# Kernel optimization log

Measured on AMD Instinct MI355X. Metric: run time of the kernel, lower is better.

The kernel has to match this reference:

```python
import jax, jax.numpy as jnp
import numpy as np

EPS = 1e-12  # torch F.normalize eps

def _l2norm(v):
    return v / jnp.maximum(jnp.linalg.norm(v, axis=-1, keepdims=True), EPS)

def setup_inputs() -> dict:
    key = jax.random.key(0)
    x = jax.random.normal(key, (64, 64, 10, 512), dtype=jnp.float32)
    w = jnp.asarray(10.0, dtype=jnp.float32)
    b = jnp.asarray(-5.0, dtype=jnp.float32)
    return {"x": x, "w": w, "b": b}

def reference(x, w, b):
    B, N, M, D = x.shape
    NM = N * M
    x_flat = _l2norm(x.reshape(B, NM, D))                      # [B, NM, D]
    c_full = _l2norm(jnp.mean(x, axis=2))                      # [B, N, D]
    # leave-one-out centroid: (M * normalized_full_centroid - x) / (M - 1), then normalize
    c_excl = _l2norm(((M * c_full[:, :, None, :] - x) / (M - 1)).reshape(B, NM, D))  # [B, NM, D]
    # cosine sim of each utterance vs every (normalized) full centroid
    sim = jnp.einsum("bkd,bnd->bkn", x_flat, c_full)           # [B, NM, N]
    # replace own-speaker column with leave-one-out similarity (avoids [B,NM,N,D] blowup)
    excl_sim = jnp.sum(x_flat * c_excl, axis=-1)               # [B, NM]
    speaker_ids = jnp.repeat(jnp.arange(N), M)                 # [NM]
    rows = jnp.arange(NM)
    sim = sim.at[:, rows, speaker_ids].set(excl_sim)
    logits = w * sim + b                                       # [B, NM, N]
    logp = jax.nn.log_softmax(logits, axis=-1)
    # cross-entropy with targets = speaker_ids per row, mean over B*NM
    nll = -logp[:, rows, speaker_ids]                          # [B, NM]
    return jnp.mean(nll)
```

## Files before the change

kernel.cpp:

```cpp
#include <hip/hip_runtime.h>
#include <math.h>

static constexpr int Bn = 64;
static constexpr int Nn = 64;
static constexpr int Mn = 10;
static constexpr int Dn = 512;
static constexpr int NMn = Nn * Mn;
static constexpr int RT = 32;
static constexpr int NBLK2 = Bn * (NMn / RT);
static constexpr float EPSV = 1e-12f;

typedef unsigned short u16;
typedef unsigned int u32;
typedef __attribute__((ext_vector_type(8))) __bf16 bf16x8;
typedef __attribute__((ext_vector_type(4))) float f32x4;

static __device__ __forceinline__ u16 f2bf(float f) {
  u32 u = __float_as_uint(f);
  u = u + 0x7fffu + ((u >> 16) & 1u);
  return (u16)(u >> 16);
}


__global__ __launch_bounds__(256) void centroid_k(const float* __restrict__ x,
                                                  u16* __restrict__ ch2) {
  const int bn = blockIdx.x;
  const int tid = threadIdx.x;
  const int f4 = tid & 127;
  const int mg = tid >> 7;
  const int wv = tid >> 6, ln = tid & 63;
  const float4* xp = (const float4*)(x + (size_t)bn * (Mn * Dn));

  float4 a = {0.f, 0.f, 0.f, 0.f};
#pragma unroll
  for (int k = 0; k < 5; ++k) {
    const float4 v = xp[(2 * k + mg) * 128 + f4];
    a.x += v.x; a.y += v.y; a.z += v.z; a.w += v.w;
  }
  __shared__ float4 cred[128];
  if (mg == 1) cred[f4] = a;
  __syncthreads();

  float4 c = {0.f, 0.f, 0.f, 0.f};
  float cs = 0.f;
  if (mg == 0) {
    c = cred[f4];
    c.x += a.x; c.y += a.y; c.z += a.z; c.w += a.w;
    cs = c.x * c.x + c.y * c.y + c.z * c.z + c.w * c.w;
  }
#pragma unroll
  for (int t = 1; t < 64; t <<= 1) cs += __shfl_xor(cs, t, 64);
  __shared__ float csred[2];
  if (mg == 0 && ln == 0) csred[wv] = cs;
  __syncthreads();
  if (mg == 0) {
    const float scale = 1.0f / fmaxf(sqrtf(csred[0] + csred[1]), EPSV);
    const u16 h0 = f2bf(c.x * scale), h1 = f2bf(c.y * scale);
    const u16 h2 = f2bf(c.z * scale), h3 = f2bf(c.w * scale);
    uint2 w;
    w.x = (u32)h0 | ((u32)h1 << 16);
    w.y = (u32)h2 | ((u32)h3 << 16);
    const int n = bn & (Nn - 1), bb = bn >> 6;
    const size_t off = (((size_t)bb * 16 + (f4 >> 3)) * Nn + n) * 32 + ((f4 & 7) * 4);
    *(uint2*)(ch2 + off) = w;
  }
}

__global__ __launch_bounds__(512) void gemm_loss_k(const float* __restrict__ x,
                                                   const u16* __restrict__ ch2,
                                                   const float* __restrict__ wp,
                                                   const float* __restrict__ bp,
                                                   float* __restrict__ partial) {
  __shared__ float S[8][16][65];
  __shared__ float SQ[2][4][16];
  __shared__ float nred[8];

  const int b = blockIdx.x / (NMn / RT);
  const int rt = blockIdx.x % (NMn / RT);
  const int row0 = rt * RT;
  const int tid = threadIdx.x, wv = tid >> 6, ln = tid & 63;
  const int lr = ln & 15;
  const int lkb = (ln >> 4) * 8;
  const int rh = wv >> 2;
  const int q = wv & 3;
  const int k0 = q * 128;

  const float* arow = x + ((size_t)b * NMn + row0 + rh * 16 + lr) * Dn + k0 + lkb;
  const u16* brow = ch2 + (((size_t)b * 16 + q * 4) * Nn) * 32 + (size_t)lr * 32 + lkb;

  f32x4 acc0 = {0.f, 0.f, 0.f, 0.f};
  f32x4 acc1 = acc0, acc2 = acc0, acc3 = acc0;
  float sq = 0.f;

#pragma unroll
  for (int kk = 0; kk < 128; kk += 32) {
    const u16* bp8 = brow + (size_t)(kk >> 5) * (Nn * 32);
    const float4 f0 = *(const float4*)(arow + kk);
    const float4 f1 = *(const float4*)(arow + kk + 4);
    const bf16x8 b0 = *(const bf16x8*)(bp8);
    const bf16x8 b1 = *(const bf16x8*)(bp8 + 16 * 32);
    const bf16x8 b2 = *(const bf16x8*)(bp8 + 32 * 32);
    const bf16x8 b3 = *(const bf16x8*)(bp8 + 48 * 32);
    const float v[8] = {f0.x, f0.y, f0.z, f0.w, f1.x, f1.y, f1.z, f1.w};
    bf16x8 ah;
#pragma unroll
    for (int i = 0; i < 8; ++i) {
      ah[i] = (__bf16)v[i];
      sq = fmaf(v[i], v[i], sq);
    }
    acc0 = __builtin_amdgcn_mfma_f32_16x16x32_bf16(ah, b0, acc0, 0, 0, 0);
    acc1 = __builtin_amdgcn_mfma_f32_16x16x32_bf16(ah, b1, acc1, 0, 0, 0);
    acc2 = __builtin_amdgcn_mfma_f32_16x16x32_bf16(ah, b2, acc2, 0, 0, 0);
    acc3 = __builtin_amdgcn_mfma_f32_16x16x32_bf16(ah, b3, acc3, 0, 0, 0);
  }

  sq += __shfl_xor(sq, 16, 64);
  sq += __shfl_xor(sq, 32, 64);
  if (ln < 16) SQ[rh][q][lr] = sq;

  const int orow = (ln >> 4) * 4;
#pragma unroll
  for (int r = 0; r < 4; ++r) {
    S[wv][orow + r][lr] = acc0[r];
    S[wv][orow + r][16 + lr] = acc1[r];
    S[wv][orow + r][32 + lr] = acc2[r];
    S[wv][orow + r][48 + lr] = acc3[r];
  }
  __syncthreads();

  const float W = *wp, Bb = *bp;
  float acc_nll = 0.f;
#pragma unroll
  for (int i = 0; i < 4; ++i) {
    const int R = wv * 4 + i;
    const int rhh = R >> 4, rl = R & 15;
    const int krow = row0 + R;
    const int spk = krow / Mn;
    const float rn = S[rhh * 4 + 0][rl][ln] + S[rhh * 4 + 1][rl][ln] +
                     S[rhh * 4 + 2][rl][ln] + S[rhh * 4 + 3][rl][ln];
    const float x2 = SQ[rhh][0][rl] + SQ[rhh][1][rl] + SQ[rhh][2][rl] + SQ[rhh][3][rl];
    const float xn = sqrtf(x2);
    const float inv_xn = 1.0f / fmaxf(xn, EPSV);
    const float rspk = __shfl(rn, spk, 64);
    float sv = rn * inv_xn;
    if (ln == spk) {
      const float num = (float)Mn * rspk - x2;
      const float en = sqrtf(fmaxf((float)(Mn * Mn) - 2.0f * (float)Mn * rspk + x2, 0.f));
      sv = num / fmaxf(xn * en, EPSV);
    }
    const float logit = W * sv + Bb;
    const float lspk = __shfl(logit, spk, 64);
    float mx = logit;
#pragma unroll
    for (int t = 1; t < 64; t <<= 1) mx = fmaxf(mx, __shfl_xor(mx, t, 64));
    float se = expf(logit - mx);
#pragma unroll
    for (int t = 1; t < 64; t <<= 1) se += __shfl_xor(se, t, 64);
    acc_nll += (mx + logf(se)) - lspk;
  }
  if (ln == 0) nred[wv] = acc_nll;
  __syncthreads();
  if (tid == 0) {
    float s = 0.f;
#pragma unroll
    for (int i = 0; i < 8; ++i) s += nred[i];
    partial[blockIdx.x] = s;
  }
}

__global__ __launch_bounds__(256) void reduce_k(const float* __restrict__ partial,
                                                float* __restrict__ out) {
  const int tid = threadIdx.x;
  float s = 0.f;
  for (int i = tid; i < NBLK2; i += 256) s += partial[i];
#pragma unroll
  for (int t = 1; t < 64; t <<= 1) s += __shfl_xor(s, t, 64);
  __shared__ float red[4];
  if ((tid & 63) == 0) red[tid >> 6] = s;
  __syncthreads();
  if (tid == 0) out[0] = (red[0] + red[1] + red[2] + red[3]) * (1.0f / (float)(Bn * NMn));
}

static constexpr int ROWS = 8;
static constexpr int DCHUNK = 128;
static constexpr int CPAD = DCHUNK + 1;

__global__ __launch_bounds__(256) void centroid_fb_k(const float* __restrict__ x,
                                                     float* __restrict__ c) {
  const int bn = blockIdx.x;
  const float* xp = x + (size_t)bn * Mn * Dn;
  const int tid = threadIdx.x;
  float a0 = 0.f, a1 = 0.f;
#pragma unroll
  for (int m = 0; m < Mn; ++m) {
    a0 += xp[m * Dn + tid];
    a1 += xp[m * Dn + tid + 256];
  }
  float s = a0 * a0 + a1 * a1;
#pragma unroll
  for (int m = 1; m < 64; m <<= 1) s += __shfl_xor(s, m, 64);
  __shared__ float red[4];
  const int wv = tid >> 6, ln = tid & 63;
  if (ln == 0) red[wv] = s;
  __syncthreads();
  const float tot = red[0] + red[1] + red[2] + red[3];
  const float scale = 1.0f / fmaxf(sqrtf(tot), EPSV);
  float* cp = c + (size_t)bn * Dn;
  cp[tid] = a0 * scale;
  cp[tid + 256] = a1 * scale;
}

__global__ __launch_bounds__(256) void loss_fb_k(const float* __restrict__ x,
                                                 const float* __restrict__ c,
                                                 const float* __restrict__ wp,
                                                 const float* __restrict__ bp,
                                                 float* __restrict__ out) {
  __shared__ __align__(16) float x_lds[ROWS * Dn];
  __shared__ float c_lds[Nn * CPAD];
  __shared__ float xn2s[ROWS];
  __shared__ float sim_lds[ROWS][Nn];

  const int tid = threadIdx.x;
  const int b = blockIdx.x / (NMn / ROWS);
  const int rblk = blockIdx.x % (NMn / ROWS);
  const int row0 = rblk * ROWS;
  const float* xrow = x + ((size_t)b * NMn + row0) * Dn;
  {
    const float4* xs = (const float4*)xrow;
    float4* xd = (float4*)x_lds;
#pragma unroll
    for (int i = tid; i < ROWS * Dn / 4; i += 256) xd[i] = xs[i];
  }
  __syncthreads();
  const int wv = tid >> 6, ln = tid & 63;
  for (int r = wv; r < ROWS; r += 4) {
    float s = 0.f;
#pragma unroll
    for (int j = ln; j < Dn; j += 64) {
      const float v = x_lds[r * Dn + j];
      s += v * v;
    }
#pragma unroll
    for (int m = 1; m < 64; m <<= 1) s += __shfl_xor(s, m, 64);
    if (ln == 0) xn2s[r] = s;
  }
  const int n = tid & 63;
  const int rg = tid >> 6;
  const int r0 = rg * 2, r1 = rg * 2 + 1;
  float s0 = 0.f, s1 = 0.f;
  const float* cb_base = c + (size_t)b * Nn * Dn;
  for (int cb = 0; cb < Dn; cb += DCHUNK) {
    __syncthreads();
    for (int i = tid; i < Nn * DCHUNK; i += 256) {
      const int nn = i / DCHUNK;
      const int j = i & (DCHUNK - 1);
      c_lds[nn * CPAD + j] = cb_base[(size_t)nn * Dn + cb + j];
    }
    __syncthreads();
#pragma unroll 16
    for (int j = 0; j < DCHUNK; ++j) {
      const float cv = c_lds[n * CPAD + j];
      s0 = fmaf(x_lds[r0 * Dn + cb + j], cv, s0);
      s1 = fmaf(x_lds[r1 * Dn + cb + j], cv, s1);
    }
  }
  sim_lds[r0][n] = s0;
  sim_lds[r1][n] = s1;
  __syncthreads();
  const float W = *wp, Bb = *bp;
  float acc_nll = 0.f;
  for (int r = wv; r < ROWS; r += 4) {
    const int k = row0 + r;
    const int spk = k / Mn;
    const float rn = sim_lds[r][ln];
    const float x2 = xn2s[r];
    const float xn = sqrtf(x2);
    const float inv_xn = 1.0f / fmaxf(xn, EPSV);
    const float rspk = sim_lds[r][spk];
    float sv = rn * inv_xn;
    if (ln == spk) {
      const float num = (float)Mn * rspk - x2;
      const float en = sqrtf(fmaxf((float)(Mn * Mn) - 2.0f * (float)Mn * rspk + x2, 0.f));
      sv = num / fmaxf(xn * en, EPSV);
    }
    const float logit = W * sv + Bb;
    const float lspk = __shfl(logit, spk, 64);
    float mx = logit;
#pragma unroll
    for (int m = 1; m < 64; m <<= 1) mx = fmaxf(mx, __shfl_xor(mx, m, 64));
    float se = expf(logit - mx);
#pragma unroll
    for (int m = 1; m < 64; m <<= 1) se += __shfl_xor(se, m, 64);
    acc_nll += (mx + logf(se)) - lspk;
  }
  __shared__ float nred[4];
  if (ln == 0) nred[wv] = acc_nll;
  __syncthreads();
  if (tid == 0)
    atomicAdd(out, (nred[0] + nred[1] + nred[2] + nred[3]) * (1.0f / (float)(Bn * NMn)));
}

extern "C" void kernel_launch(void* const* d_in, const int* in_sizes, int n_in,
                              void* d_out, int out_size, void* d_ws, size_t ws_size,
                              hipStream_t stream) {
  const float* x = (const float*)d_in[0];
  const float* w = (const float*)d_in[1];
  const float* b = (const float*)d_in[2];
  float* out = (float*)d_out;

  const size_t CSZ = (size_t)Bn * Nn * Dn * sizeof(u16);
  const size_t PSZ = (size_t)NBLK2 * sizeof(float);
  const size_t NEED = CSZ + PSZ;

  if (ws_size >= NEED) {
    char* p = (char*)d_ws;
    u16* ch2 = (u16*)p;     p += CSZ;
    float* partial = (float*)p;
    hipLaunchKernelGGL(centroid_k, dim3(Bn * Nn), dim3(256), 0, stream, x, ch2);
    hipLaunchKernelGGL(gemm_loss_k, dim3(NBLK2), dim3(512), 0, stream,
                       x, ch2, w, b, partial);
    hipLaunchKernelGGL(reduce_k, dim3(1), dim3(256), 0, stream, partial, out);
  } else {
    float* c = (float*)d_ws;
    hipMemsetAsync(out, 0, sizeof(float), stream);
    hipLaunchKernelGGL(centroid_fb_k, dim3(Bn * Nn), dim3(256), 0, stream, x, c);
    hipLaunchKernelGGL(loss_fb_k, dim3(Bn * (NMn / ROWS)), dim3(256), 0, stream,
                       x, c, w, b, out);
  }
}
```

Measured before the change: 46.24 us.

## Precompute bf16 tiled x and row norms in prep kernel, fuse final reduction via atomics

The centroid kernel now also writes a bf16 copy of x in an MFMA-friendly tiled layout, plus per-row squared norms. The gemm kernel then reads half-size bf16 operands instead of converting fp32 x. The separate reduce kernel is replaced by an atomicAdd into the output, which is zeroed in the prep kernel. This adds a 42MB write and depends on the prep kernel zeroing the output before any atomics, which stream ordering guarantees.

Result: slower. 51.95 us (+12.4%).

```diff
diff --git a/kernel.cpp b/kernel.cpp
--- a/kernel.cpp
+++ b/kernel.cpp
@@ -22,24 +22,56 @@
 }
 
 
-__global__ __launch_bounds__(256) void centroid_k(const float* __restrict__ x,
-                                                  u16* __restrict__ ch2) {
+__global__ __launch_bounds__(256) void prep_k(const float* __restrict__ x,
+                                              u16* __restrict__ ch2,
+                                              u16* __restrict__ xbf,
+                                              float* __restrict__ xn2,
+                                              float* __restrict__ out) {
   const int bn = blockIdx.x;
   const int tid = threadIdx.x;
   const int f4 = tid & 127;
   const int mg = tid >> 7;
   const int wv = tid >> 6, ln = tid & 63;
+  const int b = bn >> 6, n = bn & 63;
   const float4* xp = (const float4*)(x + (size_t)bn * (Mn * Dn));
+  const int kblk = f4 >> 3;
+  const int koff = (f4 & 7) * 4;
+
+  if (bn == 0 && tid == 0) out[0] = 0.f;
 
   float4 a = {0.f, 0.f, 0.f, 0.f};
+  float sq[5];
 #pragma unroll
   for (int k = 0; k < 5; ++k) {
-    const float4 v = xp[(2 * k + mg) * 128 + f4];
+    const int m = 2 * k + mg;
+    const float4 v = xp[m * 128 + f4];
     a.x += v.x; a.y += v.y; a.z += v.z; a.w += v.w;
+    sq[k] = v.x * v.x + v.y * v.y + v.z * v.z + v.w * v.w;
+    const u16 h0 = f2bf(v.x), h1 = f2bf(v.y), h2 = f2bf(v.z), h3 = f2bf(v.w);
+    uint2 wd;
+    wd.x = (u32)h0 | ((u32)h1 << 16);
+    wd.y = (u32)h2 | ((u32)h3 << 16);
+    const size_t off = (((size_t)b * 16 + kblk) * NMn + n * Mn + m) * 32 + koff;
+    *(uint2*)(xbf + off) = wd;
+  }
+#pragma unroll
+  for (int k = 0; k < 5; ++k) {
+#pragma unroll
+    for (int t = 1; t < 64; t <<= 1) sq[k] += __shfl_xor(sq[k], t, 64);
+  }
+  __shared__ float sqred[4][5];
+  if (ln == 0) {
+#pragma unroll
+    for (int k = 0; k < 5; ++k) sqred[wv][k] = sq[k];
   }
   __shared__ float4 cred[128];
   if (mg == 1) cred[f4] = a;
   __syncthreads();
+
+  if (tid < Mn) {
+    const int par = tid & 1, k = tid >> 1;
+    xn2[(size_t)bn * Mn + tid] = sqred[2 * par][k] + sqred[2 * par + 1][k];
+  }
 
   float4 c = {0.f, 0.f, 0.f, 0.f};
   float cs = 0.f;
@@ -60,19 +92,18 @@
     uint2 w;
     w.x = (u32)h0 | ((u32)h1 << 16);
     w.y = (u32)h2 | ((u32)h3 << 16);
-    const int n = bn & (Nn - 1), bb = bn >> 6;
-    const size_t off = (((size_t)bb * 16 + (f4 >> 3)) * Nn + n) * 32 + ((f4 & 7) * 4);
+    const size_t off = (((size_t)b * 16 + kblk) * Nn + n) * 32 + koff;
     *(uint2*)(ch2 + off) = w;
   }
 }
 
-__global__ __launch_bounds__(512) void gemm_loss_k(const float* __restrict__ x,
+__global__ __launch_bounds__(512) void gemm_loss_k(const u16* __restrict__ xbf,
                                                    const u16* __restrict__ ch2,
+                                                   const float* __restrict__ xn2,
                                                    const float* __restrict__ wp,
                                                    const float* __restrict__ bp,
-                                                   float* __restrict__ partial) {
+                                                   float* __restrict__ out) {
   __shared__ float S[8][16][65];
-  __shared__ float SQ[2][4][16];
   __shared__ float nred[8];
 
   const int b = blockIdx.x / (NMn / RT);
@@ -83,40 +114,26 @@
   const int lkb = (ln >> 4) * 8;
   const int rh = wv >> 2;
   const int q = wv & 3;
-  const int k0 = q * 128;
-
-  const float* arow = x + ((size_t)b * NMn + row0 + rh * 16 + lr) * Dn + k0 + lkb;
-  const u16* brow = ch2 + (((size_t)b * 16 + q * 4) * Nn) * 32 + (size_t)lr * 32 + lkb;
+
+  const u16* arow = xbf + (((size_t)b * 16 + q * 4) * NMn + row0 + rh * 16 + lr) * 32 + lkb;
+  const u16* brow = ch2 + (((size_t)b * 16 + q * 4) * Nn + lr) * 32 + lkb;
 
   f32x4 acc0 = {0.f, 0.f, 0.f, 0.f};
   f32x4 acc1 = acc0, acc2 = acc0, acc3 = acc0;
-  float sq = 0.f;
-
-#pragma unroll
-  for (int kk = 0; kk < 128; kk += 32) {
-    const u16* bp8 = brow + (size_t)(kk >> 5) * (Nn * 32);
-    const float4 f0 = *(const float4*)(arow + kk);
-    const float4 f1 = *(const float4*)(arow + kk + 4);
+
+#pragma unroll
+  for (int kk = 0; kk < 4; ++kk) {
+    const bf16x8 aa = *(const bf16x8*)(arow + (size_t)kk * (NMn * 32));
+    const u16* bp8 = brow + (size_t)kk * (Nn * 32);
     const bf16x8 b0 = *(const bf16x8*)(bp8);
     const bf16x8 b1 = *(const bf16x8*)(bp8 + 16 * 32);
     const bf16x8 b2 = *(const bf16x8*)(bp8 + 32 * 32);
     const bf16x8 b3 = *(const bf16x8*)(bp8 + 48 * 32);
-    const float v[8] = {f0.x, f0.y, f0.z, f0.w, f1.x, f1.y, f1.z, f1.w};
-    bf16x8 ah;
-#pragma unroll
-    for (int i = 0; i < 8; ++i) {
-      ah[i] = (__bf16)v[i];
-      sq = fmaf(v[i], v[i], sq);
-    }
-    acc0 = __builtin_amdgcn_mfma_f32_16x16x32_bf16(ah, b0, acc0, 0, 0, 0);
-    acc1 = __builtin_amdgcn_mfma_f32_16x16x32_bf16(ah, b1, acc1, 0, 0, 0);
-    acc2 = __builtin_amdgcn_mfma_f32_16x16x32_bf16(ah, b2, acc2, 0, 0, 0);
-    acc3 = __builtin_amdgcn_mfma_f32_16x16x32_bf16(ah, b3, acc3, 0, 0, 0);
-  }
-
-  sq += __shfl_xor(sq, 16, 64);
-  sq += __shfl_xor(sq, 32, 64);
-  if (ln < 16) SQ[rh][q][lr] = sq;
+    acc0 = __builtin_amdgcn_mfma_f32_16x16x32_bf16(aa, b0, acc0, 0, 0, 0);
+    acc1 = __builtin_amdgcn_mfma_f32_16x16x32_bf16(aa, b1, acc1, 0, 0, 0);
+    acc2 = __builtin_amdgcn_mfma_f32_16x16x32_bf16(aa, b2, acc2, 0, 0, 0);
+    acc3 = __builtin_amdgcn_mfma_f32_16x16x32_bf16(aa, b3, acc3, 0, 0, 0);
+  }
 
   const int orow = (ln >> 4) * 4;
 #pragma unroll
@@ -138,7 +155,7 @@
     const int spk = krow / Mn;
     const float rn = S[rhh * 4 + 0][rl][ln] + S[rhh * 4 + 1][rl][ln] +
                      S[rhh * 4 + 2][rl][ln] + S[rhh * 4 + 3][rl][ln];
-    const float x2 = SQ[rhh][0][rl] + SQ[rhh][1][rl] + SQ[rhh][2][rl] + SQ[rhh][3][rl];
+    const float x2 = xn2[(size_t)b * NMn + krow];
     const float xn = sqrtf(x2);
     const float inv_xn = 1.0f / fmaxf(xn, EPSV);
     const float rspk = __shfl(rn, spk, 64);
@@ -164,21 +181,8 @@
     float s = 0.f;
 #pragma unroll
     for (int i = 0; i < 8; ++i) s += nred[i];
-    partial[blockIdx.x] = s;
-  }
-}
-
-__global__ __launch_bounds__(256) void reduce_k(const float* __restrict__ partial,
-                                                float* __restrict__ out) {
-  const int tid = threadIdx.x;
-  float s = 0.f;
-  for (int i = tid; i < NBLK2; i += 256) s += partial[i];
-#pragma unroll
-  for (int t = 1; t < 64; t <<= 1) s += __shfl_xor(s, t, 64);
-  __shared__ float red[4];
-  if ((tid & 63) == 0) red[tid >> 6] = s;
-  __syncthreads();
-  if (tid == 0) out[0] = (red[0] + red[1] + red[2] + red[3]) * (1.0f / (float)(Bn * NMn));
+    atomicAdd(out, s * (1.0f / (float)(Bn * NMn)));
+  }
 }
 
 static constexpr int ROWS = 8;
@@ -308,18 +312,20 @@
   const float* b = (const float*)d_in[2];
   float* out = (float*)d_out;
 
-  const size_t CSZ = (size_t)Bn * Nn * Dn * sizeof(u16);
-  const size_t PSZ = (size_t)NBLK2 * sizeof(float);
-  const size_t NEED = CSZ + PSZ;
+  const size_t XSZ = (size_t)Bn * 16 * NMn * 32 * sizeof(u16);
+  const size_t CSZ = (size_t)Bn * 16 * Nn * 32 * sizeof(u16);
+  const size_t NSZ = (size_t)Bn * NMn * sizeof(float);
+  const size_t NEED = XSZ + CSZ + NSZ;
 
   if (ws_size >= NEED) {
     char* p = (char*)d_ws;
+    u16* xbf = (u16*)p;     p += XSZ;
     u16* ch2 = (u16*)p;     p += CSZ;
-    float* partial = (float*)p;
-    hipLaunchKernelGGL(centroid_k, dim3(Bn * Nn), dim3(256), 0, stream, x, ch2);
+    float* xn2 = (float*)p;
+    hipLaunchKernelGGL(prep_k, dim3(Bn * Nn), dim3(256), 0, stream,
+                       x, ch2, xbf, xn2, out);
     hipLaunchKernelGGL(gemm_loss_k, dim3(NBLK2), dim3(512), 0, stream,
-                       x, ch2, w, b, partial);
-    hipLaunchKernelGGL(reduce_k, dim3(1), dim3(256), 0, stream, partial, out);
+                       xbf, ch2, xn2, w, b, out);
   } else {
     float* c = (float*)d_ws;
     hipMemsetAsync(out, 0, sizeof(float), stream);
```
